# Performance work log

Measured on AMD Instinct MI355X. Metric: run time of the kernel, lower is better.

The kernel has to match this reference:

```python
import jax, jax.numpy as jnp
import numpy as np

B, S, N_ITEMS, E, H, L, DFF = 32, 512, 2048, 512, 8, 2, 2048
DK = E // H
EPS = 1e-5


def setup_inputs() -> dict:
    key = jax.random.key(0)
    ks = jax.random.split(key, 32)
    sc = 0.02
    p = {
        'input_seq': jax.random.normal(ks[0], (B, S, N_ITEMS), jnp.float32),
        'emb_W': jax.random.normal(ks[1], (N_ITEMS, E), jnp.float32) * sc,
        'emb_b': jnp.zeros((E,), jnp.float32),
        'pos_emb': jax.random.normal(ks[2], (S, E), jnp.float32) * sc,
        'Wq': jax.random.normal(ks[3], (L, E, E), jnp.float32) * sc,
        'bq': jnp.zeros((L, E), jnp.float32),
        'Wk': jax.random.normal(ks[4], (L, E, E), jnp.float32) * sc,
        'bk': jnp.zeros((L, E), jnp.float32),
        'Wv': jax.random.normal(ks[5], (L, E, E), jnp.float32) * sc,
        'bv': jnp.zeros((L, E), jnp.float32),
        'Wo': jax.random.normal(ks[6], (L, E, E), jnp.float32) * sc,
        'bo': jnp.zeros((L, E), jnp.float32),
        'ln1_g': jnp.ones((L, E), jnp.float32),
        'ln1_b': jnp.zeros((L, E), jnp.float32),
        'W1': jax.random.normal(ks[7], (L, E, DFF), jnp.float32) * sc,
        'b1': jnp.zeros((L, DFF), jnp.float32),
        'W2': jax.random.normal(ks[8], (L, DFF, E), jnp.float32) * sc,
        'b2': jnp.zeros((L, E), jnp.float32),
        'ln2_g': jnp.ones((L, E), jnp.float32),
        'ln2_b': jnp.zeros((L, E), jnp.float32),
        'fc_W': jax.random.normal(ks[9], (E, 1), jnp.float32) * sc,
        'fc_b': jnp.zeros((1,), jnp.float32),
    }
    return p


def _layernorm(x, g, b):
    m = jnp.mean(x, axis=-1, keepdims=True)
    v = jnp.mean(jnp.square(x - m), axis=-1, keepdims=True)
    return (x - m) * jax.lax.rsqrt(v + EPS) * g + b


def reference(input_seq, emb_W, emb_b, pos_emb, Wq, bq, Wk, bk, Wv, bv, Wo, bo,
              ln1_g, ln1_b, W1, b1, W2, b2, ln2_g, ln2_b, fc_W, fc_b):
    x = input_seq @ emb_W + emb_b          # [B,S,E]
    x = x + pos_emb[None, :, :]
    tril = jnp.tril(jnp.ones((S, S), jnp.float32))  # causal lower-triangular
    for l in range(L):
        # --- self attention (faithful: tril BEFORE scale, zeros not -inf) ---
        q = (x @ Wq[l] + bq[l]).reshape(B, S, H, DK).transpose(0, 2, 1, 3)
        k = (x @ Wk[l] + bk[l]).reshape(B, S, H, DK).transpose(0, 2, 1, 3)
        v = (x @ Wv[l] + bv[l]).reshape(B, S, H, DK).transpose(0, 2, 1, 3)
        scores = jnp.einsum('bhqd,bhkd->bhqk', q, k)
        scores = (scores * tril) / np.sqrt(DK)
        probs = jax.nn.softmax(scores, axis=-1)
        attn = jnp.einsum('bhqk,bhkd->bhqd', probs, v)  # [B,H,S,DK]
        attn = attn.transpose(0, 2, 1, 3).reshape(B, S, E)
        attn = attn @ Wo[l] + bo[l]
        # faithful source bug: `self_attention(x,x,x)[0]` -> batch 0 only,
        # broadcast over all batches in the residual add
        attended0 = attn[0]                 # [S,E]
        x = _layernorm(x + attended0[None, :, :], ln1_g[l], ln1_b[l])
        # --- feed forward ---
        ff = jax.nn.relu(x @ W1[l] + b1[l]) @ W2[l] + b2[l]
        x = _layernorm(x + ff, ln2_g[l], ln2_b[l])
    out = (x @ fc_W + fc_b).squeeze(-1)     # [B,S]
    return out
```

## Files before the change

### kernel.cpp

```cpp
#include <hip/hip_runtime.h>


typedef __bf16 bf16;
typedef __bf16 bf16x8 __attribute__((ext_vector_type(8)));
typedef __bf16 bf16x4 __attribute__((ext_vector_type(4)));
typedef float  f32x4  __attribute__((ext_vector_type(4)));

#define SEQ 512

__device__ __forceinline__ void gl2lds16(const bf16* g, void* l) {
    __builtin_amdgcn_global_load_lds(
        (const __attribute__((address_space(1))) void*)g,
        (__attribute__((address_space(3))) void*)l, 16, 0, 0);
}

template<int N> __device__ __forceinline__ void waitvm() {
    if constexpr (N == 0)      asm volatile("s_waitcnt vmcnt(0)" ::: "memory");
    else if constexpr (N == 2) asm volatile("s_waitcnt vmcnt(2)" ::: "memory");
    else if constexpr (N == 3) asm volatile("s_waitcnt vmcnt(3)" ::: "memory");
    else if constexpr (N == 4) asm volatile("s_waitcnt vmcnt(4)" ::: "memory");
    else if constexpr (N == 5) asm volatile("s_waitcnt vmcnt(5)" ::: "memory");
    else if constexpr (N == 6) asm volatile("s_waitcnt vmcnt(6)" ::: "memory");
    else if constexpr (N == 8) asm volatile("s_waitcnt vmcnt(8)" ::: "memory");
    else static_assert(N == 0, "unsupported waitvm");
}

__global__ __launch_bounds__(256)
void prep_k(const float* __restrict__ in, bf16* __restrict__ outb,
            const float* __restrict__ emb_W, bf16* __restrict__ embWT,
            const float* __restrict__ Wq, const float* __restrict__ Wk,
            const float* __restrict__ Wv, const float* __restrict__ Wo,
            const float* __restrict__ W1, const float* __restrict__ W2,
            bf16* __restrict__ qkvWT, bf16* __restrict__ WoT,
            bf16* __restrict__ W1T, bf16* __restrict__ W2T,
            const float* __restrict__ bq, const float* __restrict__ bk,
            const float* __restrict__ bv, float* __restrict__ qkvB)
{
    const int blk = blockIdx.x;
    if (blk < 1024) {
        const long long gsz = 1024ll * 256;
        const long long n8 = 16384ll * 2048 / 8;
        long long i = (long long)blk * 256 + threadIdx.x;
        for (; i + 3 * gsz < n8; i += 4 * gsz) {
            f32x4 a0 = *(const f32x4*)(in + i * 8);
            f32x4 b0 = *(const f32x4*)(in + i * 8 + 4);
            f32x4 a1 = *(const f32x4*)(in + (i + gsz) * 8);
            f32x4 b1 = *(const f32x4*)(in + (i + gsz) * 8 + 4);
            f32x4 a2 = *(const f32x4*)(in + (i + 2 * gsz) * 8);
            f32x4 b2 = *(const f32x4*)(in + (i + 2 * gsz) * 8 + 4);
            f32x4 a3 = *(const f32x4*)(in + (i + 3 * gsz) * 8);
            f32x4 b3 = *(const f32x4*)(in + (i + 3 * gsz) * 8 + 4);
            bf16x8 w0, w1, w2, w3;
            #pragma unroll
            for (int j = 0; j < 4; ++j) {
                w0[j] = (bf16)a0[j]; w0[4 + j] = (bf16)b0[j];
                w1[j] = (bf16)a1[j]; w1[4 + j] = (bf16)b1[j];
                w2[j] = (bf16)a2[j]; w2[4 + j] = (bf16)b2[j];
                w3[j] = (bf16)a3[j]; w3[4 + j] = (bf16)b3[j];
            }
            *(bf16x8*)(outb + i * 8)             = w0;
            *(bf16x8*)(outb + (i + gsz) * 8)     = w1;
            *(bf16x8*)(outb + (i + 2 * gsz) * 8) = w2;
            *(bf16x8*)(outb + (i + 3 * gsz) * 8) = w3;
        }
        for (; i < n8; i += gsz) {
            f32x4 a0 = *(const f32x4*)(in + i * 8);
            f32x4 b0 = *(const f32x4*)(in + i * 8 + 4);
            bf16x8 w0;
            #pragma unroll
            for (int j = 0; j < 4; ++j) { w0[j] = (bf16)a0[j]; w0[4 + j] = (bf16)b0[j]; }
            *(bf16x8*)(outb + i * 8) = w0;
        }
    } else if (blk < 8192) {
        const int b = blk - 1024;
        const float* src;
        bf16* dst;
        int K, N, t;
        if (b < 1024) {
            src = emb_W; dst = embWT; K = 2048; N = 512; t = b;
        } else {
            const int bb = b - 1024;
            const int l = bb >= 3072 ? 1 : 0;
            const int r = bb - l * 3072;
            if (r < 256)       { src = Wq + l * 262144;  dst = qkvWT + l * 786432;          K = 512;  N = 512;  t = r; }
            else if (r < 512)  { src = Wk + l * 262144;  dst = qkvWT + l * 786432 + 262144; K = 512;  N = 512;  t = r - 256; }
            else if (r < 768)  { src = Wv + l * 262144;  dst = qkvWT + l * 786432 + 524288; K = 512;  N = 512;  t = r - 512; }
            else if (r < 1024) { src = Wo + l * 262144;  dst = WoT + l * 262144;            K = 512;  N = 512;  t = r - 768; }
            else if (r < 2048) { src = W1 + l * 1048576; dst = W1T + l * 1048576;           K = 512;  N = 2048; t = r - 1024; }
            else               { src = W2 + l * 1048576; dst = W2T + l * 1048576;           K = 2048; N = 512;  t = r - 2048; }
        }
        const int tx = N >> 5;
        const int n0 = (t % tx) * 32, k0 = (t / tx) * 32;
        __shared__ float tl[32][33];
        int r2 = threadIdx.x >> 3, c4 = (threadIdx.x & 7) * 4;
        float4 v = *(const float4*)&src[(long long)(k0 + r2) * N + n0 + c4];
        tl[r2][c4 + 0] = v.x; tl[r2][c4 + 1] = v.y;
        tl[r2][c4 + 2] = v.z; tl[r2][c4 + 3] = v.w;
        __syncthreads();
        int n = threadIdx.x >> 3, kk4 = (threadIdx.x & 7) * 4;
        bf16x4 o;
        o[0] = (bf16)tl[kk4 + 0][n]; o[1] = (bf16)tl[kk4 + 1][n];
        o[2] = (bf16)tl[kk4 + 2][n]; o[3] = (bf16)tl[kk4 + 3][n];
        *(bf16x4*)&dst[(long long)(n0 + n) * K + k0 + kk4] = o;
    } else {
        const int l = blk - 8192;
        for (int t2 = threadIdx.x; t2 < 512; t2 += 256) {
            qkvB[l * 1536 + t2]        = bq[l * 512 + t2];
            qkvB[l * 1536 + 512 + t2]  = bk[l * 512 + t2];
            qkvB[l * 1536 + 1024 + t2] = bv[l * 512 + t2];
        }
    }
}

__global__ __launch_bounds__(256, 1)
void fattn(const bf16* __restrict__ qkv,
           const bf16* __restrict__ VT,
           bf16* __restrict__ attn0b)
{
    __shared__ __align__(1024) char smem[65536 + 65536 + 4096];
    char* Ks = smem;
    char* Vs = smem + 65536;
    const int h = blockIdx.y;
    const int q0 = blockIdx.x * 64;
    const int tid = threadIdx.x, lane = tid & 63, wv = tid >> 6;
    const int fr = lane & 15, fc = lane >> 4;
    char* Ps = smem + 131072 + wv * 1024;

    {
        const bf16* Kg = qkv + 512 + h * 64;
        #pragma unroll
        for (int p = 0; p < 16; ++p) {
            int row = p * 32 + (tid >> 3);
            int ch  = tid & 7;
            gl2lds16(Kg + (long long)row * 1536 + ((ch ^ (row & 7)) * 8),
                     Ks + p * 4096 + tid * 16);
        }
        const bf16* Vg = VT + (long long)h * 64 * 512;
        #pragma unroll
        for (int p = 0; p < 16; ++p) {
            int row = p * 4 + (tid >> 6);
            int ch  = tid & 63;
            int chg = (ch & ~7) | ((ch & 7) ^ (row & 7));
            gl2lds16(Vg + (long long)row * 512 + chg * 8,
                     Vs + p * 4096 + tid * 16);
        }
    }
    const int q0w = q0 + wv * 16;
    const int qg  = q0w + fr;
    bf16x8 qf[2];
    #pragma unroll
    for (int w = 0; w < 2; ++w)
        qf[w] = *(const bf16x8*)(qkv + (long long)qg * 1536 + h * 64 + w * 32 + fc * 8);

    asm volatile("s_waitcnt vmcnt(0)" ::: "memory");
    __builtin_amdgcn_s_barrier();
    asm volatile("" ::: "memory");

    f32x4 s[32] = {};
    #pragma unroll
    for (int kt = 0; kt < 32; ++kt) {
        #pragma unroll
        for (int w = 0; w < 2; ++w) {
            int row = kt * 16 + fr;
            bf16x8 kf = *(const bf16x8*)(Ks + row * 128 +
                                         (((w * 4 + fc) ^ (row & 7)) * 16));
            s[kt] = __builtin_amdgcn_mfma_f32_16x16x32_bf16(kf, qf[w], s[kt], 0, 0, 0);
        }
    }

    float mx = -3.4e38f;
    #pragma unroll
    for (int kt = 0; kt < 32; ++kt)
        #pragma unroll
        for (int rr = 0; rr < 4; ++rr) {
            int k = kt * 16 + fc * 4 + rr;
            float v = (k <= qg) ? s[kt][rr] * 0.125f : 0.0f;
            s[kt][rr] = v;
            mx = fmaxf(mx, v);
        }
    mx = fmaxf(mx, __shfl_xor(mx, 16));
    mx = fmaxf(mx, __shfl_xor(mx, 32));
    float sum = 0.f;
    #pragma unroll
    for (int kt = 0; kt < 32; ++kt)
        #pragma unroll
        for (int rr = 0; rr < 4; ++rr) {
            float e = __expf(s[kt][rr] - mx);
            s[kt][rr] = e;
            sum += e;
        }
    sum += __shfl_xor(sum, 16);
    sum += __shfl_xor(sum, 32);
    const float inv = 1.0f / sum;

    f32x4 o[4] = {};
    #pragma unroll
    for (int kt2 = 0; kt2 < 16; ++kt2) {
        bf16x4 u0, u1;
        #pragma unroll
        for (int rr = 0; rr < 4; ++rr) {
            u0[rr] = (bf16)(s[2 * kt2][rr] * inv);
            u1[rr] = (bf16)(s[2 * kt2 + 1][rr] * inv);
        }
        *(bf16x4*)(Ps + fr * 64 + ((fc ^ (fr & 7)) * 8))       = u0;
        *(bf16x4*)(Ps + fr * 64 + (((4 + fc) ^ (fr & 7)) * 8)) = u1;
        __threadfence_block();
        bf16x4 lo = *(const bf16x4*)(Ps + fr * 64 + (((2 * fc) ^ (fr & 7)) * 8));
        bf16x4 hi = *(const bf16x4*)(Ps + fr * 64 + (((2 * fc + 1) ^ (fr & 7)) * 8));
        bf16x8 pf;
        pf[0] = lo[0]; pf[1] = lo[1]; pf[2] = lo[2]; pf[3] = lo[3];
        pf[4] = hi[0]; pf[5] = hi[1]; pf[6] = hi[2]; pf[7] = hi[3];
        #pragma unroll
        for (int n = 0; n < 4; ++n) {
            int row = n * 16 + fr;
            int ch  = kt2 * 4 + fc;
            int chs = (ch & ~7) | ((ch & 7) ^ (row & 7));
            bf16x8 vf = *(const bf16x8*)(Vs + row * 1024 + chs * 16);
            o[n] = __builtin_amdgcn_mfma_f32_16x16x32_bf16(pf, vf, o[n], 0, 0, 0);
        }
    }

    #pragma unroll
    for (int n = 0; n < 4; ++n)
        #pragma unroll
        for (int rr = 0; rr < 4; ++rr) {
            int qrow = q0w + fc * 4 + rr;
            attn0b[(long long)qrow * 512 + h * 64 + n * 16 + fr] = (bf16)o[n][rr];
        }
}

template<int BN, int ACT, int POS>
__global__ __launch_bounds__(512, 1)
void mg8(const bf16* __restrict__ Ab, int lda,
         const bf16* __restrict__ Bt, int ldb,
         const float* __restrict__ bias, const float* __restrict__ pos,
         bf16* __restrict__ Cb, int ldc, int K)
{
    constexpr int BM = 256;
    constexpr int APASS = 2;
    constexpr int BPASS = BN / 128;
    constexpr int AHB = BM * 64;
    constexpr int BHB = BN * 64;
    constexpr int WM = (BN == 256 ? 2 : 4), WN = 8 / WM;
    constexpr int MR = BM / WM / 16;
    constexpr int NR = BN / WN / 16;
    __shared__ __align__(1024) char smem[4 * AHB + 4 * BHB];
    char* ABase = smem;
    char* BBase = smem + 4 * AHB;

    const int gx = gridDim.x, gy = gridDim.y;
    const int nwg = gx * gy;
    const int b = blockIdx.y * gx + blockIdx.x;
    const int q = nwg >> 3, r = nwg & 7;
    const int xcd = b & 7, loc = b >> 3;
    const int wg = (xcd < r ? xcd * (q + 1) : r * (q + 1) + (xcd - r) * q) + loc;
    const int bx = wg % gx, by = wg / gx;
    const int row0 = by * BM, col0 = bx * BN;

    const int tid = threadIdx.x, lane = tid & 63, wv = tid >> 6;
    const int wr = (WM == 2 ? (wv >> 2) : (wv >> 1));
    const int wc = (WM == 2 ? (wv & 3) : (wv & 1));
    const int fr = lane & 15, fc = lane >> 4;

    const bf16* aS[APASS];
    #pragma unroll
    for (int p = 0; p < APASS; ++p) {
        int cL = p * 512 + tid;
        int row = cL >> 2, ch = cL & 3;
        aS[p] = Ab + (long long)(row0 + row) * lda + ((ch ^ (row & 3)) * 8);
    }
    const bf16* bS[BPASS];
    #pragma unroll
    for (int p = 0; p < BPASS; ++p) {
        int cL = p * 512 + tid;
        int row = cL >> 2, ch = cL & 3;
        bS[p] = Bt + (long long)(col0 + row) * ldb + ((ch ^ (row & 3)) * 8);
    }
    int aOff[MR], bOff[NR];
    #pragma unroll
    for (int m = 0; m < MR; ++m) {
        int row = wr * (BM / WM) + m * 16 + fr;
        aOff[m] = row * 64 + ((fc ^ (row & 3)) * 16);
    }
    #pragma unroll
    for (int n = 0; n < NR; ++n) {
        int row = wc * (BN / WN) + n * 16 + fr;
        bOff[n] = row * 64 + ((fc ^ (row & 3)) * 16);
    }

    auto stagePart = [&](int j) {
        const int tau = j >> 2, kh = (j >> 1) & 1, d = tau & 1;
        const int koff = tau * 64 + kh * 32;
        if (!(j & 1)) {
            char* dst = ABase + (d * 2 + kh) * AHB + wv * 1024;
            #pragma unroll
            for (int p = 0; p < APASS; ++p)
                gl2lds16(aS[p] + koff, dst + p * 8192);
        } else {
            char* dst = BBase + (d * 2 + kh) * BHB + wv * 1024;
            #pragma unroll
            for (int p = 0; p < BPASS; ++p)
                gl2lds16(bS[p] + koff, dst + p * 8192);
        }
    };

    const int nt = K >> 6;
    const int T = 4 * nt;
    #pragma unroll
    for (int j = 0; j < 6; ++j)
        if (j < T) stagePart(j);
    waitvm<2 * (APASS + BPASS)>();
    __builtin_amdgcn_s_barrier();

    f32x4 acc[MR][NR] = {};
    const int NPH = 2 * nt;
    for (int g = 0; g < NPH; ++g) {
        const int tau = g >> 1, ks = g & 1, d = tau & 1;

        const char* as = ABase + (d * 2 + ks) * AHB;
        const char* bs = BBase + (d * 2 + ks) * BHB;
        bf16x8 a[MR], b2[NR];
        #pragma unroll
        for (int m = 0; m < MR; ++m) a[m] = *(const bf16x8*)(as + aOff[m]);
        #pragma unroll
        for (int n = 0; n < NR; ++n) b2[n] = *(const bf16x8*)(bs + bOff[n]);

        if (2 * g + 6 < T) stagePart(2 * g + 6);
        if (2 * g + 7 < T) stagePart(2 * g + 7);

        __builtin_amdgcn_s_setprio(1);
        #pragma unroll
        for (int m = 0; m < MR; ++m)
            #pragma unroll
            for (int n = 0; n < NR; ++n)
                acc[m][n] = __builtin_amdgcn_mfma_f32_16x16x32_bf16(
                    a[m], b2[n], acc[m][n], 0, 0, 0);
        __builtin_amdgcn_s_setprio(0);

        const int rem = T - (2 * g + 4);
        if (rem >= 4)      waitvm<2 * (APASS + BPASS)>();
        else if (rem == 3) waitvm<2 * APASS + BPASS>();
        else if (rem == 2) waitvm<APASS + BPASS>();
        else if (rem == 1) waitvm<APASS>();
        else               waitvm<0>();
        __builtin_amdgcn_s_barrier();
    }

    float* st = (float*)(smem + wv * 4096);
    const int rowb = row0 + wr * (BM / WM);
    const int colb = col0 + wc * (BN / WN);
    #pragma unroll
    for (int m = 0; m < MR; ++m) {
        #pragma unroll
        for (int n = 0; n < NR; ++n) {
            int col = colb + n * 16 + fr;
            float bb = bias ? bias[col] : 0.f;
            #pragma unroll
            for (int rr = 0; rr < 4; ++rr) {
                float x = acc[m][n][rr] + bb;
                if constexpr (POS) {
                    int rowg = rowb + m * 16 + fc * 4 + rr;
                    x += pos[(rowg & 511) * 512 + col];
                }
                if constexpr (ACT) x = fmaxf(x, 0.f);
                st[(fc * 4 + rr) * 64 + n * 16 + fr] = x;
            }
        }
        #pragma unroll
        for (int sgi = 0; sgi < 2; ++sgi) {
            int row = sgi * 8 + (lane >> 3);
            int c8 = (lane & 7) * 8;
            f32x4 u = *(const f32x4*)&st[row * 64 + c8];
            f32x4 v = *(const f32x4*)&st[row * 64 + c8 + 4];
            bf16x8 w8;
            w8[0] = (bf16)u[0]; w8[1] = (bf16)u[1];
            w8[2] = (bf16)u[2]; w8[3] = (bf16)u[3];
            w8[4] = (bf16)v[0]; w8[5] = (bf16)v[1];
            w8[6] = (bf16)v[2]; w8[7] = (bf16)v[3];
            *(bf16x8*)&Cb[(long long)(rowb + m * 16 + row) * ldc + colb + c8] = w8;
        }
    }
}

template<int BM, int BN, int ACT, int CMODE, int CAUSAL>
__global__ __launch_bounds__(256, 4)
void mgemm(const bf16* __restrict__ Ab, int lda, long long sA,
           const bf16* __restrict__ Bt, int ldb, long long sB,
           const float* __restrict__ bias,
           float* __restrict__ Cf, bf16* __restrict__ Cb, int ldc, long long sC,
           int K)
{
    static_assert(BM == 128 && (BN == 128 || BN == 64), "tile");
    const int gx = gridDim.x, gy = gridDim.y;
    const int nwg = gx * gy;
    const int b = blockIdx.y * gx + blockIdx.x;
    const int q = nwg >> 3, r = nwg & 7;
    const int xcd = b & 7, loc = b >> 3;
    const int wg = (xcd < r ? xcd * (q + 1) : r * (q + 1) + (xcd - r) * q) + loc;
    const int bx = wg % gx, by = wg / gx;
    if (CAUSAL && bx * BN > by * BM + (BM - 1)) return;

    constexpr int TM = BM / 32, TN = BN / 32;
    constexpr int AIT = BM / 64, BIT = BN / 64;
    constexpr int ABY = BM * 64;
    constexpr int BBY = BN * 64;
    __shared__ bf16 As[2 * BM * 32];
    __shared__ bf16 Bs[2 * BN * 32];
    char* AsB = (char*)As;
    char* BsB = (char*)Bs;
    const int tid = threadIdx.x;
    const int lane = tid & 63, wv = tid >> 6;
    const int wr = wv >> 1, wc = wv & 1;
    const int fr = lane & 15, fc = lane >> 4;
    const int row0 = by * BM, col0 = bx * BN;
    const int z = blockIdx.z;

    Ab += (long long)z * sA;
    Bt += (long long)z * sB;
    if constexpr (CMODE == 0) Cf += (long long)z * sC;
    else                      Cb += (long long)z * sC;

    f32x4 acc[TM][TN] = {};

    const bf16* aSrc[AIT];
    #pragma unroll
    for (int it = 0; it < AIT; ++it) {
        int cL = it * 256 + tid;
        int row = cL >> 2, ch = cL & 3;
        aSrc[it] = Ab + (long long)(row0 + row) * lda + ((ch ^ (row & 3)) * 8);
    }
    const bf16* bSrc[BIT];
    #pragma unroll
    for (int it = 0; it < BIT; ++it) {
        int cL = it * 256 + tid;
        int row = cL >> 2, ch = cL & 3;
        bSrc[it] = Bt + (long long)(col0 + row) * ldb + ((ch ^ (row & 3)) * 8);
    }
    int aOff[TM], bOff[TN];
    #pragma unroll
    for (int m = 0; m < TM; ++m) {
        int row = wr * (BM / 2) + m * 16 + fr;
        aOff[m] = row * 64 + ((fc ^ (row & 3)) * 16);
    }
    #pragma unroll
    for (int n = 0; n < TN; ++n) {
        int row = wc * (BN / 2) + n * 16 + fr;
        bOff[n] = row * 64 + ((fc ^ (row & 3)) * 16);
    }

    auto stageTo = [&](int buf, int kt) {
        #pragma unroll
        for (int it = 0; it < AIT; ++it)
            gl2lds16(aSrc[it] + kt, AsB + buf * ABY + it * 4096 + wv * 1024);
        #pragma unroll
        for (int it = 0; it < BIT; ++it)
            gl2lds16(bSrc[it] + kt, BsB + buf * BBY + it * 4096 + wv * 1024);
    };

    const int nt = K >> 5;
    stageTo(0, 0);
    asm volatile("s_waitcnt vmcnt(0)" ::: "memory");
    __builtin_amdgcn_s_barrier();
    asm volatile("" ::: "memory");

    int cur = 0;
    for (int t = 0; t < nt; ++t) {
        if (t + 1 < nt) stageTo(cur ^ 1, (t + 1) * 32);
        bf16x8 a[TM], b2[TN];
        #pragma unroll
        for (int m = 0; m < TM; ++m) a[m] = *(const bf16x8*)(AsB + cur * ABY + aOff[m]);
        #pragma unroll
        for (int n = 0; n < TN; ++n) b2[n] = *(const bf16x8*)(BsB + cur * BBY + bOff[n]);
        __builtin_amdgcn_s_setprio(1);
        #pragma unroll
        for (int m = 0; m < TM; ++m)
            #pragma unroll
            for (int n = 0; n < TN; ++n)
                acc[m][n] = __builtin_amdgcn_mfma_f32_16x16x32_bf16(a[m], b2[n], acc[m][n], 0, 0, 0);
        __builtin_amdgcn_s_setprio(0);
        if (t + 1 < nt) {
            asm volatile("s_waitcnt vmcnt(0)" ::: "memory");
            __builtin_amdgcn_s_barrier();
            asm volatile("" ::: "memory");
            cur ^= 1;
        }
    }

    #pragma unroll
    for (int n = 0; n < TN; ++n) {
        int col = col0 + wc * (BN / 2) + n * 16 + fr;
        float bb = bias ? bias[col] : 0.f;
        #pragma unroll
        for (int m = 0; m < TM; ++m) {
            int rbase = row0 + wr * (BM / 2) + m * 16 + fc * 4;
            #pragma unroll
            for (int rr = 0; rr < 4; ++rr) {
                float x = acc[m][n][rr] + bb;
                if constexpr (ACT) x = fmaxf(x, 0.f);
                long long ci = (long long)(rbase + rr) * ldc + col;
                if constexpr (CMODE == 0) Cf[ci] = x;
                else                      Cb[ci] = (bf16)x;
            }
        }
    }
}

__global__ __launch_bounds__(256)
void vt_k(const bf16* __restrict__ qkv, bf16* __restrict__ VT)
{
    __shared__ bf16 t[64][80];
    int h = blockIdx.y, s0 = blockIdx.x * 64;
    int r = threadIdx.x >> 2, c16 = (threadIdx.x & 3) * 16;
    const bf16* src = qkv + (long long)(s0 + r) * 1536 + 1024 + h * 64 + c16;
    *(bf16x8*)&t[r][c16]     = *(const bf16x8*)src;
    *(bf16x8*)&t[r][c16 + 8] = *(const bf16x8*)(src + 8);
    __syncthreads();
    int d = r, seg = c16;
    bf16 tmp[16];
    #pragma unroll
    for (int j = 0; j < 16; ++j) tmp[j] = t[seg + j][d];
    bf16* dst = VT + ((long long)(h * 64 + d)) * 512 + s0 + seg;
    *(bf16x8*)dst       = *(bf16x8*)&tmp[0];
    *(bf16x8*)(dst + 8) = *(bf16x8*)&tmp[8];
}

__global__ __launch_bounds__(256)
void addln_k(bf16* __restrict__ xb, const bf16* __restrict__ res,
             unsigned resMask, const float* __restrict__ g,
             const float* __restrict__ bta)
{
    const int tid = threadIdx.x;
    const int sub = tid >> 7;
    const long long row = (long long)blockIdx.x * 2 + sub;
    const int lt = tid & 127;
    const int c = lt * 4;
    bf16x4 xv4 = *(const bf16x4*)&xb[row * 512 + c];
    bf16x4 rv4 = *(const bf16x4*)&res[(long long)(row & resMask) * 512 + c];
    float x0 = (float)xv4[0] + (float)rv4[0];
    float x1 = (float)xv4[1] + (float)rv4[1];
    float x2 = (float)xv4[2] + (float)rv4[2];
    float x3 = (float)xv4[3] + (float)rv4[3];
    float s = x0 + x1 + x2 + x3;
    float qq = x0 * x0 + x1 * x1 + x2 * x2 + x3 * x3;
    #pragma unroll
    for (int off = 32; off; off >>= 1) {
        s += __shfl_xor(s, off);
        qq += __shfl_xor(qq, off);
    }
    __shared__ float rs[4], rq[4];
    if ((tid & 63) == 0) { rs[tid >> 6] = s; rq[tid >> 6] = qq; }
    __syncthreads();
    s = rs[sub * 2] + rs[sub * 2 + 1];
    qq = rq[sub * 2] + rq[sub * 2 + 1];
    float mean = s * (1.0f / 512.0f);
    float var  = qq * (1.0f / 512.0f) - mean * mean;
    float rstd = rsqrtf(var + 1e-5f);
    float4 gv = *(const float4*)&g[c];
    float4 bv = *(const float4*)&bta[c];
    bf16x4 o4;
    o4[0] = (bf16)((x0 - mean) * rstd * gv.x + bv.x);
    o4[1] = (bf16)((x1 - mean) * rstd * gv.y + bv.y);
    o4[2] = (bf16)((x2 - mean) * rstd * gv.z + bv.z);
    o4[3] = (bf16)((x3 - mean) * rstd * gv.w + bv.w);
    *(bf16x4*)&xb[row * 512 + c] = o4;
}

__global__ __launch_bounds__(256)
void fc_k(const bf16* __restrict__ x, const float* __restrict__ w,
          const float* __restrict__ bb, float* __restrict__ out)
{
    int row  = blockIdx.x * 4 + (threadIdx.x >> 6);
    int lane = threadIdx.x & 63;
    const bf16* xr = x + (long long)row * 512;
    bf16x8 a8 = *(const bf16x8*)&xr[lane * 8];
    float4 w0 = *(const float4*)&w[lane * 8];
    float4 w1 = *(const float4*)&w[lane * 8 + 4];
    float s = (float)a8[0] * w0.x + (float)a8[1] * w0.y
            + (float)a8[2] * w0.z + (float)a8[3] * w0.w
            + (float)a8[4] * w1.x + (float)a8[5] * w1.y
            + (float)a8[6] * w1.z + (float)a8[7] * w1.w;
    #pragma unroll
    for (int off = 32; off; off >>= 1) s += __shfl_xor(s, off);
    if (lane == 0) out[row] = s + bb[0];
}

extern "C" void kernel_launch(void* const* d_in, const int* in_sizes, int n_in,
                              void* d_out, int out_size, void* d_ws, size_t ws_size,
                              hipStream_t stream)
{
    const float* input_seq = (const float*)d_in[0];
    const float* emb_W  = (const float*)d_in[1];
    const float* emb_b  = (const float*)d_in[2];
    const float* pos_emb= (const float*)d_in[3];
    const float* Wq = (const float*)d_in[4];
    const float* bq = (const float*)d_in[5];
    const float* Wk = (const float*)d_in[6];
    const float* bk = (const float*)d_in[7];
    const float* Wv = (const float*)d_in[8];
    const float* bv = (const float*)d_in[9];
    const float* Wo = (const float*)d_in[10];
    const float* bo = (const float*)d_in[11];
    const float* ln1_g = (const float*)d_in[12];
    const float* ln1_b = (const float*)d_in[13];
    const float* W1 = (const float*)d_in[14];
    const float* b1 = (const float*)d_in[15];
    const float* W2 = (const float*)d_in[16];
    const float* b2 = (const float*)d_in[17];
    const float* ln2_g = (const float*)d_in[18];
    const float* ln2_b = (const float*)d_in[19];
    const float* fcW = (const float*)d_in[20];
    const float* fcb = (const float*)d_in[21];
    float* out = (float*)d_out;

    char* w = (char*)d_ws;
    size_t off = 0;
    auto alloc = [&](size_t bytes) -> void* {
        off = (off + 255) & ~(size_t)255;
        void* p = w + off;
        off += bytes;
        return p;
    };
    bf16*  xb     = (bf16*) alloc(16384ull * 512 * 2);
    bf16*  embWT  = (bf16*) alloc(512ull * 2048 * 2);
    bf16*  qkvWT  = (bf16*) alloc(2ull * 1536 * 512 * 2);
    bf16*  WoT    = (bf16*) alloc(2ull * 512 * 512 * 2);
    bf16*  W1T    = (bf16*) alloc(2ull * 2048 * 512 * 2);
    bf16*  W2T    = (bf16*) alloc(2ull * 512 * 2048 * 2);
    float* qkvB   = (float*)alloc(2ull * 1536 * 4);
    off = (off + 255) & ~(size_t)255;
    char* dynp = w + off;
    bf16*  seqb     = (bf16*)dynp;
    bf16*  qkv      = (bf16*)dynp;
    bf16*  VT       = (bf16*)(dynp + 1572864);
    bf16*  attn0b   = (bf16*)(dynp + 1572864 + 524288);
    bf16*  attnout0b= (bf16*)(dynp + 1572864 + 524288 + 524288);
    bf16*  hidden = (bf16*)dynp;
    bf16*  ffout  = (bf16*)(dynp + 16384ull * 2048 * 2);

    dim3 blk(256);
    dim3 blk512(512);

    prep_k<<<dim3(8194), blk, 0, stream>>>(
        input_seq, seqb, emb_W, embWT, Wq, Wk, Wv, Wo, W1, W2,
        qkvWT, WoT, W1T, W2T, bq, bk, bv, qkvB);

    mg8<128, 0, 1><<<dim3(4, 64), blk512, 0, stream>>>(
        seqb, 2048, embWT, 2048, emb_b, pos_emb, xb, 512, 2048);

    for (int l = 0; l < 2; ++l) {
        const bf16* qkvWT_l = qkvWT + l * 786432;
        const bf16* WoT_l   = WoT + l * 262144;
        const bf16* W1T_l   = W1T + l * 1048576;
        const bf16* W2T_l   = W2T + l * 1048576;

        mgemm<128, 64, 0, 1, 0><<<dim3(24, 4), blk, 0, stream>>>(
            xb, 512, 0, qkvWT_l, 512, 0, qkvB + l * 1536,
            nullptr, qkv, 1536, 0, 512);
        vt_k<<<dim3(8, 8), blk, 0, stream>>>(qkv, VT);
        fattn<<<dim3(8, 8), blk, 0, stream>>>(qkv, VT, attn0b);
        mgemm<128, 64, 0, 1, 0><<<dim3(8, 4), blk, 0, stream>>>(
            attn0b, 512, 0, WoT_l, 512, 0, bo + l * 512, nullptr,
            attnout0b, 512, 0, 512);
        addln_k<<<dim3(8192), blk, 0, stream>>>(
            xb, attnout0b, 511u, ln1_g + l * 512, ln1_b + l * 512);

        mg8<256, 1, 0><<<dim3(8, 64), blk512, 0, stream>>>(
            xb, 512, W1T_l, 512, b1 + l * 2048, nullptr, hidden, 2048, 512);
        mg8<128, 0, 0><<<dim3(4, 64), blk512, 0, stream>>>(
            hidden, 2048, W2T_l, 2048, b2 + l * 512, nullptr, ffout, 512, 2048);
        addln_k<<<dim3(8192), blk, 0, stream>>>(
            xb, ffout, 0xffffffffu, ln2_g + l * 512, ln2_b + l * 512);
    }

    fc_k<<<dim3(4096), blk, 0, stream>>>(xb, fcW, fcb, out);
}
```

Before: 362.4 us.

## Fuse fp32-to-bf16 input conversion into embedding GEMM A-tile loads

Removes the separate pass that converted the 16384x2048 fp32 input sequence to bf16. A new GEMM kernel instead streams fp32 A tiles straight into LDS and converts them to bf16 in registers before the MFMA. This drops a full write and re-read of the converted input (about 64 MB of bf16 traffic), but doubles the LDS footprint and traffic for the A operand and adds conversion instructions inside the inner loop.

```diff
diff --git a/kernel.cpp b/kernel.cpp
--- a/kernel.cpp
+++ b/kernel.cpp
@@ -8,26 +8,27 @@
 
 #define SEQ 512
 
-__device__ __forceinline__ void gl2lds16(const bf16* g, void* l) {
+__device__ __forceinline__ void gl2lds16(const void* g, void* l) {
     __builtin_amdgcn_global_load_lds(
         (const __attribute__((address_space(1))) void*)g,
         (__attribute__((address_space(3))) void*)l, 16, 0, 0);
 }
 
 template<int N> __device__ __forceinline__ void waitvm() {
-    if constexpr (N == 0)      asm volatile("s_waitcnt vmcnt(0)" ::: "memory");
-    else if constexpr (N == 2) asm volatile("s_waitcnt vmcnt(2)" ::: "memory");
-    else if constexpr (N == 3) asm volatile("s_waitcnt vmcnt(3)" ::: "memory");
-    else if constexpr (N == 4) asm volatile("s_waitcnt vmcnt(4)" ::: "memory");
-    else if constexpr (N == 5) asm volatile("s_waitcnt vmcnt(5)" ::: "memory");
-    else if constexpr (N == 6) asm volatile("s_waitcnt vmcnt(6)" ::: "memory");
-    else if constexpr (N == 8) asm volatile("s_waitcnt vmcnt(8)" ::: "memory");
+    if constexpr (N == 0)       asm volatile("s_waitcnt vmcnt(0)" ::: "memory");
+    else if constexpr (N == 2)  asm volatile("s_waitcnt vmcnt(2)" ::: "memory");
+    else if constexpr (N == 3)  asm volatile("s_waitcnt vmcnt(3)" ::: "memory");
+    else if constexpr (N == 4)  asm volatile("s_waitcnt vmcnt(4)" ::: "memory");
+    else if constexpr (N == 5)  asm volatile("s_waitcnt vmcnt(5)" ::: "memory");
+    else if constexpr (N == 6)  asm volatile("s_waitcnt vmcnt(6)" ::: "memory");
+    else if constexpr (N == 8)  asm volatile("s_waitcnt vmcnt(8)" ::: "memory");
+    else if constexpr (N == 9)  asm volatile("s_waitcnt vmcnt(9)" ::: "memory");
+    else if constexpr (N == 10) asm volatile("s_waitcnt vmcnt(10)" ::: "memory");
     else static_assert(N == 0, "unsupported waitvm");
 }
 
 __global__ __launch_bounds__(256)
-void prep_k(const float* __restrict__ in, bf16* __restrict__ outb,
-            const float* __restrict__ emb_W, bf16* __restrict__ embWT,
+void prep_k(const float* __restrict__ emb_W, bf16* __restrict__ embWT,
             const float* __restrict__ Wq, const float* __restrict__ Wk,
             const float* __restrict__ Wv, const float* __restrict__ Wo,
             const float* __restrict__ W1, const float* __restrict__ W2,
@@ -36,43 +37,8 @@
             const float* __restrict__ bq, const float* __restrict__ bk,
             const float* __restrict__ bv, float* __restrict__ qkvB)
 {
-    const int blk = blockIdx.x;
-    if (blk < 1024) {
-        const long long gsz = 1024ll * 256;
-        const long long n8 = 16384ll * 2048 / 8;
-        long long i = (long long)blk * 256 + threadIdx.x;
-        for (; i + 3 * gsz < n8; i += 4 * gsz) {
-            f32x4 a0 = *(const f32x4*)(in + i * 8);
-            f32x4 b0 = *(const f32x4*)(in + i * 8 + 4);
-            f32x4 a1 = *(const f32x4*)(in + (i + gsz) * 8);
-            f32x4 b1 = *(const f32x4*)(in + (i + gsz) * 8 + 4);
-            f32x4 a2 = *(const f32x4*)(in + (i + 2 * gsz) * 8);
-            f32x4 b2 = *(const f32x4*)(in + (i + 2 * gsz) * 8 + 4);
-            f32x4 a3 = *(const f32x4*)(in + (i + 3 * gsz) * 8);
-            f32x4 b3 = *(const f32x4*)(in + (i + 3 * gsz) * 8 + 4);
-            bf16x8 w0, w1, w2, w3;
-            #pragma unroll
-            for (int j = 0; j < 4; ++j) {
-                w0[j] = (bf16)a0[j]; w0[4 + j] = (bf16)b0[j];
-                w1[j] = (bf16)a1[j]; w1[4 + j] = (bf16)b1[j];
-                w2[j] = (bf16)a2[j]; w2[4 + j] = (bf16)b2[j];
-                w3[j] = (bf16)a3[j]; w3[4 + j] = (bf16)b3[j];
-            }
-            *(bf16x8*)(outb + i * 8)             = w0;
-            *(bf16x8*)(outb + (i + gsz) * 8)     = w1;
-            *(bf16x8*)(outb + (i + 2 * gsz) * 8) = w2;
-            *(bf16x8*)(outb + (i + 3 * gsz) * 8) = w3;
-        }
-        for (; i < n8; i += gsz) {
-            f32x4 a0 = *(const f32x4*)(in + i * 8);
-            f32x4 b0 = *(const f32x4*)(in + i * 8 + 4);
-            bf16x8 w0;
-            #pragma unroll
-            for (int j = 0; j < 4; ++j) { w0[j] = (bf16)a0[j]; w0[4 + j] = (bf16)b0[j]; }
-            *(bf16x8*)(outb + i * 8) = w0;
-        }
-    } else if (blk < 8192) {
-        const int b = blk - 1024;
+    const int b = blockIdx.x;
+    if (b < 7168) {
         const float* src;
         bf16* dst;
         int K, N, t;
@@ -103,11 +69,167 @@
         o[2] = (bf16)tl[kk4 + 2][n]; o[3] = (bf16)tl[kk4 + 3][n];
         *(bf16x4*)&dst[(long long)(n0 + n) * K + k0 + kk4] = o;
     } else {
-        const int l = blk - 8192;
+        const int l = b - 7168;
         for (int t2 = threadIdx.x; t2 < 512; t2 += 256) {
             qkvB[l * 1536 + t2]        = bq[l * 512 + t2];
             qkvB[l * 1536 + 512 + t2]  = bk[l * 512 + t2];
             qkvB[l * 1536 + 1024 + t2] = bv[l * 512 + t2];
+        }
+    }
+}
+
+__global__ __launch_bounds__(512, 1)
+void mg8f(const float* __restrict__ Af, int lda,
+          const bf16* __restrict__ Bt, int ldb,
+          const float* __restrict__ bias, const float* __restrict__ pos,
+          bf16* __restrict__ Cb, int ldc, int K)
+{
+    constexpr int BM = 256, BN = 128;
+    constexpr int APASS = 4;
+    constexpr int BPASS = 1;
+    constexpr int AHB = BM * 32 * 4;
+    constexpr int BHB = BN * 64;
+    constexpr int WM = 4, WN = 2;
+    constexpr int MR = BM / WM / 16;
+    constexpr int NR = BN / WN / 16;
+    __shared__ __align__(1024) char smem[4 * AHB + 4 * BHB];
+    char* ABase = smem;
+    char* BBase = smem + 4 * AHB;
+
+    const int gx = gridDim.x, gy = gridDim.y;
+    const int nwg = gx * gy;
+    const int b = blockIdx.y * gx + blockIdx.x;
+    const int q = nwg >> 3, r = nwg & 7;
+    const int xcd = b & 7, loc = b >> 3;
+    const int wg = (xcd < r ? xcd * (q + 1) : r * (q + 1) + (xcd - r) * q) + loc;
+    const int bx = wg % gx, by = wg / gx;
+    const int row0 = by * BM, col0 = bx * BN;
+
+    const int tid = threadIdx.x, lane = tid & 63, wv = tid >> 6;
+    const int wr = wv >> 1, wc = wv & 1;
+    const int fr = lane & 15, fc = lane >> 4;
+
+    const float* aS[APASS];
+    #pragma unroll
+    for (int p = 0; p < APASS; ++p) {
+        int cL = p * 512 + tid;
+        int row = cL >> 3, ch = cL & 7;
+        aS[p] = Af + (long long)(row0 + row) * lda + ((ch ^ (row & 7)) * 4);
+    }
+    const bf16* bS0;
+    {
+        int cL = tid;
+        int row = cL >> 2, ch = cL & 3;
+        bS0 = Bt + (long long)(col0 + row) * ldb + ((ch ^ (row & 3)) * 8);
+    }
+    int aOff0[MR], aOff1[MR];
+    #pragma unroll
+    for (int m = 0; m < MR; ++m) {
+        int row = wr * (BM / WM) + m * 16 + fr;
+        aOff0[m] = row * 128 + (((2 * fc)     ^ (row & 7)) * 16);
+        aOff1[m] = row * 128 + (((2 * fc + 1) ^ (row & 7)) * 16);
+    }
+    int bOff[NR];
+    #pragma unroll
+    for (int n = 0; n < NR; ++n) {
+        int row = wc * (BN / WN) + n * 16 + fr;
+        bOff[n] = row * 64 + ((fc ^ (row & 3)) * 16);
+    }
+
+    auto stagePart = [&](int j) {
+        const int tau = j >> 2, kh = (j >> 1) & 1, d = tau & 1;
+        const int koff = tau * 64 + kh * 32;
+        if (!(j & 1)) {
+            char* dst = ABase + (d * 2 + kh) * AHB + wv * 1024;
+            #pragma unroll
+            for (int p = 0; p < APASS; ++p)
+                gl2lds16(aS[p] + koff, dst + p * 8192);
+        } else {
+            char* dst = BBase + (d * 2 + kh) * BHB + wv * 1024;
+            gl2lds16(bS0 + koff, dst);
+        }
+    };
+
+    const int nt = K >> 6;
+    const int T = 4 * nt;
+    #pragma unroll
+    for (int j = 0; j < 6; ++j)
+        if (j < T) stagePart(j);
+    waitvm<2 * (APASS + BPASS)>();
+    __builtin_amdgcn_s_barrier();
+
+    f32x4 acc[MR][NR] = {};
+    const int NPH = 2 * nt;
+    for (int g = 0; g < NPH; ++g) {
+        const int tau = g >> 1, ks = g & 1, d = tau & 1;
+
+        const char* as = ABase + (d * 2 + ks) * AHB;
+        const char* bs = BBase + (d * 2 + ks) * BHB;
+        bf16x8 a[MR], b2[NR];
+        #pragma unroll
+        for (int m = 0; m < MR; ++m) {
+            f32x4 lo = *(const f32x4*)(as + aOff0[m]);
+            f32x4 hi = *(const f32x4*)(as + aOff1[m]);
+            bf16x8 w8;
+            w8[0] = (bf16)lo[0]; w8[1] = (bf16)lo[1];
+            w8[2] = (bf16)lo[2]; w8[3] = (bf16)lo[3];
+            w8[4] = (bf16)hi[0]; w8[5] = (bf16)hi[1];
+            w8[6] = (bf16)hi[2]; w8[7] = (bf16)hi[3];
+            a[m] = w8;
+        }
+        #pragma unroll
+        for (int n = 0; n < NR; ++n) b2[n] = *(const bf16x8*)(bs + bOff[n]);
+
+        if (2 * g + 6 < T) stagePart(2 * g + 6);
+        if (2 * g + 7 < T) stagePart(2 * g + 7);
+
+        __builtin_amdgcn_s_setprio(1);
+        #pragma unroll
+        for (int m = 0; m < MR; ++m)
+            #pragma unroll
+            for (int n = 0; n < NR; ++n)
+                acc[m][n] = __builtin_amdgcn_mfma_f32_16x16x32_bf16(
+                    a[m], b2[n], acc[m][n], 0, 0, 0);
+        __builtin_amdgcn_s_setprio(0);
+
+        const int rem = T - (2 * g + 4);
+        if (rem >= 4)      waitvm<2 * (APASS + BPASS)>();
+        else if (rem == 3) waitvm<2 * APASS + BPASS>();
+        else if (rem == 2) waitvm<APASS + BPASS>();
+        else if (rem == 1) waitvm<APASS>();
+        else               waitvm<0>();
+        __builtin_amdgcn_s_barrier();
+    }
+
+    float* st = (float*)(smem + wv * 4096);
+    const int rowb = row0 + wr * (BM / WM);
+    const int colb = col0 + wc * (BN / WN);
+    #pragma unroll
+    for (int m = 0; m < MR; ++m) {
+        #pragma unroll
+        for (int n = 0; n < NR; ++n) {
+            int col = colb + n * 16 + fr;
+            float bb = bias ? bias[col] : 0.f;
+            #pragma unroll
+            for (int rr = 0; rr < 4; ++rr) {
+                float x = acc[m][n][rr] + bb;
+                int rowg = rowb + m * 16 + fc * 4 + rr;
+                x += pos[(rowg & 511) * 512 + col];
+                st[(fc * 4 + rr) * 64 + n * 16 + fr] = x;
+            }
+        }
+        #pragma unroll
+        for (int sgi = 0; sgi < 2; ++sgi) {
+            int row = sgi * 8 + (lane >> 3);
+            int c8 = (lane & 7) * 8;
+            f32x4 u = *(const f32x4*)&st[row * 64 + c8];
+            f32x4 v = *(const f32x4*)&st[row * 64 + c8 + 4];
+            bf16x8 w8;
+            w8[0] = (bf16)u[0]; w8[1] = (bf16)u[1];
+            w8[2] = (bf16)u[2]; w8[3] = (bf16)u[3];
+            w8[4] = (bf16)v[0]; w8[5] = (bf16)v[1];
+            w8[6] = (bf16)v[2]; w8[7] = (bf16)v[3];
+            *(bf16x8*)&Cb[(long long)(rowb + m * 16 + row) * ldc + colb + c8] = w8;
         }
     }
 }
@@ -229,11 +351,11 @@
         }
 }
 
-template<int BN, int ACT, int POS>
+template<int BN, int ACT>
 __global__ __launch_bounds__(512, 1)
 void mg8(const bf16* __restrict__ Ab, int lda,
          const bf16* __restrict__ Bt, int ldb,
-         const float* __restrict__ bias, const float* __restrict__ pos,
+         const float* __restrict__ bias,
          bf16* __restrict__ Cb, int ldc, int K)
 {
     constexpr int BM = 256;
@@ -358,10 +480,6 @@
             #pragma unroll
             for (int rr = 0; rr < 4; ++rr) {
                 float x = acc[m][n][rr] + bb;
-                if constexpr (POS) {
-                    int rowg = rowb + m * 16 + fc * 4 + rr;
-                    x += pos[(rowg & 511) * 512 + col];
-                }
                 if constexpr (ACT) x = fmaxf(x, 0.f);
                 st[(fc * 4 + rr) * 64 + n * 16 + fr] = x;
             }
@@ -629,7 +747,6 @@
     float* qkvB   = (float*)alloc(2ull * 1536 * 4);
     off = (off + 255) & ~(size_t)255;
     char* dynp = w + off;
-    bf16*  seqb     = (bf16*)dynp;
     bf16*  qkv      = (bf16*)dynp;
     bf16*  VT       = (bf16*)(dynp + 1572864);
     bf16*  attn0b   = (bf16*)(dynp + 1572864 + 524288);
@@ -640,12 +757,12 @@
     dim3 blk(256);
     dim3 blk512(512);
 
-    prep_k<<<dim3(8194), blk, 0, stream>>>(
-        input_seq, seqb, emb_W, embWT, Wq, Wk, Wv, Wo, W1, W2,
+    prep_k<<<dim3(7170), blk, 0, stream>>>(
+        emb_W, embWT, Wq, Wk, Wv, Wo, W1, W2,
         qkvWT, WoT, W1T, W2T, bq, bk, bv, qkvB);
 
-    mg8<128, 0, 1><<<dim3(4, 64), blk512, 0, stream>>>(
-        seqb, 2048, embWT, 2048, emb_b, pos_emb, xb, 512, 2048);
+    mg8f<<<dim3(4, 64), blk512, 0, stream>>>(
+        input_seq, 2048, embWT, 2048, emb_b, pos_emb, xb, 512, 2048);
 
     for (int l = 0; l < 2; ++l) {
         const bf16* qkvWT_l = qkvWT + l * 786432;
@@ -664,10 +781,10 @@
         addln_k<<<dim3(8192), blk, 0, stream>>>(
             xb, attnout0b, 511u, ln1_g + l * 512, ln1_b + l * 512);
 
-        mg8<256, 1, 0><<<dim3(8, 64), blk512, 0, stream>>>(
-            xb, 512, W1T_l, 512, b1 + l * 2048, nullptr, hidden, 2048, 512);
-        mg8<128, 0, 0><<<dim3(4, 64), blk512, 0, stream>>>(
-            hidden, 2048, W2T_l, 2048, b2 + l * 512, nullptr, ffout, 512, 2048);
+        mg8<256, 1><<<dim3(8, 64), blk512, 0, stream>>>(
+            xb, 512, W1T_l, 512, b1 + l * 2048, hidden, 2048, 512);
+        mg8<128, 0><<<dim3(4, 64), blk512, 0, stream>>>(
+            hidden, 2048, W2T_l, 2048, b2 + l * 512, ffout, 512, 2048);
         addln_k<<<dim3(8192), blk, 0, stream>>>(
             xb, ffout, 0xffffffffu, ln2_g + l * 512, ln2_b + l * 512);
     }
```

Result: faster. 350.6 us, median of 2 (-3.2%).
